# Kernel tuning notes

Measured on AMD Instinct MI355X. Metric: run time of the kernel, lower is better.

The kernel has to match this reference:

```python
import jax, jax.numpy as jnp
import numpy as np

D_K = 64  # hardcoded in source module

def setup_inputs() -> dict:
    key = jax.random.key(0)
    kq, kk, kv, km = jax.random.split(key, 4)
    B, H, S, D = 4, 16, 2048, D_K
    Q = jax.random.normal(kq, (B, H, S, D), dtype=jnp.float32)
    K = jax.random.normal(kk, (B, H, S, D), dtype=jnp.float32)
    V = jax.random.normal(kv, (B, H, S, D), dtype=jnp.float32)
    attn_mask = jax.random.randint(km, (B, H, S, S), 0, 2).astype(jnp.bool_)
    return {"Q": Q, "K": K, "V": V, "attn_mask": attn_mask}

def reference(Q, K, V, attn_mask):
    # scores: [B, H, len_q, len_k]
    scores = jnp.einsum("bhqd,bhkd->bhqk", Q, K) / np.sqrt(D_K).astype(np.float32)
    scores = jnp.where(attn_mask, jnp.float32(-1e9), scores)
    attn = jax.nn.softmax(scores, axis=-1)
    prob = jnp.einsum("bhqk,bhkd->bhqd", attn, V)
    return prob, attn
```

## Files before the change

### kernel.cpp

```cpp
#include <hip/hip_runtime.h>
#include <stdint.h>

typedef _Float16 f16;
typedef _Float16 f16x8 __attribute__((ext_vector_type(8)));
typedef _Float16 f16x4 __attribute__((ext_vector_type(4)));
typedef float f32x4 __attribute__((ext_vector_type(4)));
typedef int int4v __attribute__((ext_vector_type(4)));
typedef float float4v __attribute__((ext_vector_type(4)));

#define S_LEN 2048
#define D_DIM 64
#define QBLK 128
#define KBLK 64
#define NTHREADS 512
#define KSTEPS 32

#define BARRIER() do { \
    asm volatile("s_waitcnt lgkmcnt(0)" ::: "memory"); \
    __builtin_amdgcn_s_barrier(); \
    asm volatile("" ::: "memory"); \
} while (0)

__device__ __forceinline__ f16x8 cvt8(float4v a, float4v b) {
    f16x8 f;
    f[0]=(f16)a[0]; f[1]=(f16)a[1]; f[2]=(f16)a[2]; f[3]=(f16)a[3];
    f[4]=(f16)b[0]; f[5]=(f16)b[1]; f[6]=(f16)b[2]; f[7]=(f16)b[3];
    return f;
}
__device__ __forceinline__ uint32_t f16b(float x) {
    union { f16 h; uint16_t u; } c; c.h = (f16)x; return c.u;
}

#define S1_BODY(T, MREG) do { \
    const int tt = ((T) + phase) & 31; \
    const int cur = (T) & 1; \
    BARRIER(); \
    uint32_t bits = 0; \
    _Pragma("unroll") \
    for (int ct = 0; ct < 4; ++ct) { \
        _Pragma("unroll") \
        for (int r = 0; r < 4; ++r) \
            bits |= (MREG[ct][r] != 0 ? 1u : 0u) << (4 * ct + r); \
    } \
    if ((T) + 1 < KSTEPS) {    \
        const int tn = ((T) + 1 + phase) & 31; \
        const float* kp = kbase + (size_t)(tn * KBLK + srow) * D_DIM + scol; \
        ka = *(const float4v*)kp; kb = *(const float4v*)(kp + 4); \
    } \
    if ((T) + 2 < KSTEPS) {    \
        const int tm = ((T) + 2 + phase) & 31; \
        _Pragma("unroll") \
        for (int ct = 0; ct < 4; ++ct) \
            MREG[ct] = __builtin_nontemporal_load( \
                (const int4v*)(mbase + (size_t)tm * KBLK + 16 * ct)); \
    } \
    f32x4 c[4]; \
    _Pragma("unroll") \
    for (int ct = 0; ct < 4; ++ct) { \
        c[ct] = (f32x4){0.f, 0.f, 0.f, 0.f}; \
        _Pragma("unroll") \
        for (int h = 0; h < 2; ++h) { \
            int rowl = 16 * ct + lr; \
            int idx = (rowl * D_DIM + 8 * g + 32 * h) ^ ((rowl & 7) << 3); \
            f16x8 kf = *(const f16x8*)(&Klds[cur][idx]); \
            c[ct] = __builtin_amdgcn_mfma_f32_16x16x32_f16(kf, qfrag[h], c[ct], 0, 0, 0); \
        } \
    } \
    Mw[tt][tid] = (uint16_t)bits; \
    _Pragma("unroll") \
    for (int ct = 0; ct < 4; ++ct) { \
        _Pragma("unroll") \
        for (int r = 0; r < 4; ++r) { \
            float s = c[ct][r] * 0.125f; \
            float p = ((bits >> (4 * ct + r)) & 1) ? 0.f : __expf(s);  \
            lacc[r] += p; \
        } \
    } \
    if ((T) + 1 < KSTEPS) \
        *(f16x8*)&Klds[cur ^ 1][sidx] = cvt8(ka, kb); \
} while (0)

__global__ __launch_bounds__(NTHREADS, 4)
void sdpa_kernel(const float* __restrict__ Qg, const float* __restrict__ Kg,
                 const float* __restrict__ Vg, const int* __restrict__ Mg,
                 float* __restrict__ ProbOut, float* __restrict__ AttnOut)
{
    __shared__ f16 Klds[2][KBLK * D_DIM];
    __shared__ f16 Vtlds[2][D_DIM * KBLK];
    __shared__ uint16_t Mw[KSTEPS][NTHREADS];

    const int tid  = threadIdx.x;
    const int lane = tid & 63;
    const int wq   = tid >> 6;
    const int g    = lane >> 4;
    const int lr   = lane & 15;

    const int wid = ((blockIdx.x & 7) << 7) + (blockIdx.x >> 3);
    const int bh  = wid >> 4;
    const int qb  = wid & 15;
    const int phase = ((bh & 3) << 3) | ((qb & 1) << 2);

    const size_t qkv_base = (size_t)bh * S_LEN * D_DIM;
    const size_t mat_base = (size_t)bh * S_LEN * S_LEN;
    const int qw0 = qb * QBLK + wq * 16;

    f16x8 qfrag[2];
    {
        const float* qp = Qg + qkv_base + (size_t)(qw0 + lr) * D_DIM + g * 8;
        #pragma unroll
        for (int h = 0; h < 2; ++h)
            qfrag[h] = cvt8(*(const float4v*)(qp + 32 * h),
                            *(const float4v*)(qp + 32 * h + 4));
    }

    const int srow = tid >> 3, scol = (tid & 7) * 8;
    const int sidx = (srow * D_DIM + scol) ^ ((srow & 7) << 3);
    const int vrp  = tid >> 4, vdb = (tid & 15) * 4;
    const int vk   = 2 * vrp;
    const int vkp  = (vk & 3) | (((vk >> 4) & 3) << 2) | (((vk >> 2) & 3) << 4);

    const float* kbase = Kg + qkv_base;
    const float* vbase = Vg + qkv_base;
    const int*   mbase = Mg + mat_base + (size_t)(qw0 + lr) * S_LEN + 4 * g;

    float lacc[4] = {0.f, 0.f, 0.f, 0.f};

    float4v ka, kb;
    int4v mregA[4], mregB[4];
    {
        const float* kp = kbase + (size_t)(phase * KBLK + srow) * D_DIM + scol;
        ka = *(const float4v*)kp; kb = *(const float4v*)(kp + 4);
        const int t1 = (phase + 1) & 31;
        #pragma unroll
        for (int ct = 0; ct < 4; ++ct) {
            mregA[ct] = __builtin_nontemporal_load(
                (const int4v*)(mbase + (size_t)phase * KBLK + 16 * ct));
            mregB[ct] = __builtin_nontemporal_load(
                (const int4v*)(mbase + (size_t)t1 * KBLK + 16 * ct));
        }
    }
    *(f16x8*)&Klds[0][sidx] = cvt8(ka, kb);

    for (int t2 = 0; t2 < KSTEPS; t2 += 2) {
        S1_BODY(t2, mregA);
        S1_BODY(t2 + 1, mregB);
    }

    float lsum = (lacc[0] + lacc[1]) + (lacc[2] + lacc[3]);
    lsum += __shfl_xor(lsum, 16, 64);
    lsum += __shfl_xor(lsum, 32, 64);
    const float inv_l = 1.f / lsum;

    f32x4 acc[4];
    #pragma unroll
    for (int dt = 0; dt < 4; ++dt) acc[dt] = (f32x4){0.f, 0.f, 0.f, 0.f};

    float4v va, vb;
    {
        const float* kp = kbase + (size_t)(phase * KBLK + srow) * D_DIM + scol;
        ka = *(const float4v*)kp; kb = *(const float4v*)(kp + 4);
        const float* vp = vbase + (size_t)(phase * KBLK + vk) * D_DIM + vdb;
        va = *(const float4v*)vp; vb = *(const float4v*)(vp + D_DIM);
    }
    *(f16x8*)&Klds[0][sidx] = cvt8(ka, kb);
    #pragma unroll
    for (int j = 0; j < 4; ++j) {
        int d = vdb + j;
        uint32_t pk = f16b(va[j]) | (f16b(vb[j]) << 16);
        *(uint32_t*)&Vtlds[0][(d * KBLK + vkp) ^ ((d & 7) << 3)] = pk;
    }

    for (int t = 0; t < KSTEPS; ++t) {
        const int tt  = (t + phase) & 31;
        const int cur = t & 1;
        BARRIER();
        if (t + 1 < KSTEPS) {
            const int tn = (t + 1 + phase) & 31;
            const float* kp = kbase + (size_t)(tn * KBLK + srow) * D_DIM + scol;
            ka = *(const float4v*)kp; kb = *(const float4v*)(kp + 4);
            const float* vp = vbase + (size_t)(tn * KBLK + vk) * D_DIM + vdb;
            va = *(const float4v*)vp; vb = *(const float4v*)(vp + D_DIM);
        }
        f32x4 c[4];
        #pragma unroll
        for (int ct = 0; ct < 4; ++ct) {
            c[ct] = (f32x4){0.f, 0.f, 0.f, 0.f};
            #pragma unroll
            for (int h = 0; h < 2; ++h) {
                int rowl = 16 * ct + lr;
                int idx = (rowl * D_DIM + 8 * g + 32 * h) ^ ((rowl & 7) << 3);
                f16x8 kf = *(const f16x8*)(&Klds[cur][idx]);
                c[ct] = __builtin_amdgcn_mfma_f32_16x16x32_f16(kf, qfrag[h], c[ct], 0, 0, 0);
            }
        }
        const uint32_t bits = Mw[tt][tid];
        f16x4 pa[4];
        #pragma unroll
        for (int ct = 0; ct < 4; ++ct) {
            float4v av;
            #pragma unroll
            for (int r = 0; r < 4; ++r) {
                float s = c[ct][r] * 0.125f;
                float p = ((bits >> (4 * ct + r)) & 1) ? 0.f : __expf(s);
                float pn = p * inv_l;
                av[r] = pn; pa[ct][r] = (f16)pn;
            }
            __builtin_nontemporal_store(av,
                (float4v*)(AttnOut + mat_base + (size_t)(qw0 + lr) * S_LEN
                           + tt * KBLK + 16 * ct + 4 * g));
        }
        #pragma unroll
        for (int dt = 0; dt < 4; ++dt) {
            int row = 16 * dt + lr;
            f16x8 vfA = *(const f16x8*)&Vtlds[cur][(row * KBLK + 16 * g)      ^ ((lr & 7) << 3)];
            f16x8 vfB = *(const f16x8*)&Vtlds[cur][(row * KBLK + 16 * g + 8)  ^ ((lr & 7) << 3)];
            acc[dt] = __builtin_amdgcn_mfma_f32_16x16x16f16(
                pa[0], __builtin_shufflevector(vfA, vfA, 0, 1, 2, 3), acc[dt], 0, 0, 0);
            acc[dt] = __builtin_amdgcn_mfma_f32_16x16x16f16(
                pa[1], __builtin_shufflevector(vfA, vfA, 4, 5, 6, 7), acc[dt], 0, 0, 0);
            acc[dt] = __builtin_amdgcn_mfma_f32_16x16x16f16(
                pa[2], __builtin_shufflevector(vfB, vfB, 0, 1, 2, 3), acc[dt], 0, 0, 0);
            acc[dt] = __builtin_amdgcn_mfma_f32_16x16x16f16(
                pa[3], __builtin_shufflevector(vfB, vfB, 4, 5, 6, 7), acc[dt], 0, 0, 0);
        }
        if (t + 1 < KSTEPS) {
            *(f16x8*)&Klds[cur ^ 1][sidx] = cvt8(ka, kb);
            #pragma unroll
            for (int j = 0; j < 4; ++j) {
                int d = vdb + j;
                uint32_t pk = f16b(va[j]) | (f16b(vb[j]) << 16);
                *(uint32_t*)&Vtlds[cur ^ 1][(d * KBLK + vkp) ^ ((d & 7) << 3)] = pk;
            }
        }
    }

    #pragma unroll
    for (int dt = 0; dt < 4; ++dt) {
        #pragma unroll
        for (int r = 0; r < 4; ++r) {
            int qrow = qw0 + 4 * g + r;
            ProbOut[qkv_base + (size_t)qrow * D_DIM + 16 * dt + lr] = acc[dt][r];
        }
    }
}

extern "C" void kernel_launch(void* const* d_in, const int* in_sizes, int n_in,
                              void* d_out, int out_size, void* d_ws, size_t ws_size,
                              hipStream_t stream)
{
    const float* Q = (const float*)d_in[0];
    const float* K = (const float*)d_in[1];
    const float* V = (const float*)d_in[2];
    const int*   M = (const int*)d_in[3];

    float* prob = (float*)d_out;
    float* attn = prob + (size_t)4 * 16 * 2048 * 64;

    dim3 grid(64 * (S_LEN / QBLK));
    dim3 block(NTHREADS);
    sdpa_kernel<<<grid, block, 0, stream>>>(Q, K, V, M, prob, attn);
}
```

Baseline: 585.4 us.

## Halve Q block, load K fragments directly from global and drop K LDS staging

Shrinks the workgroup to 4 waves and 64 query rows, so there are twice as many blocks, and remaps the block-to-(bh,qb) swizzle and phase. Each wave now loads its K MFMA fragments straight from global memory and converts them in registers. This removes the shared K double buffer and the barriers in the first softmax-sum pass. The risk is redundant K global traffic across waves and blocks, which must be absorbed by L2/L1, and more per-thread V loading in the second pass.

```diff
diff --git a/kernel.cpp b/kernel.cpp
--- a/kernel.cpp
+++ b/kernel.cpp
@@ -10,9 +10,9 @@
 
 #define S_LEN 2048
 #define D_DIM 64
-#define QBLK 128
+#define QBLK 64
 #define KBLK 64
-#define NTHREADS 512
+#define NTHREADS 256
 #define KSTEPS 32
 
 #define BARRIER() do { \
@@ -31,10 +31,36 @@
     union { f16 h; uint16_t u; } c; c.h = (f16)x; return c.u;
 }
 
+#define QKT_DIRECT(C, K0) do { \
+    _Pragma("unroll") \
+    for (int half = 0; half < 2; ++half) { \
+        float4v kr[8]; \
+        _Pragma("unroll") \
+        for (int cc = 0; cc < 2; ++cc) { \
+            _Pragma("unroll") \
+            for (int h = 0; h < 2; ++h) { \
+                const float* kp = kbase + (size_t)((K0) + 16 * (2 * half + cc) + lr) * D_DIM \
+                                  + 8 * g + 32 * h; \
+                kr[(cc << 2) | (h << 1)]     = *(const float4v*)kp; \
+                kr[(cc << 2) | (h << 1) | 1] = *(const float4v*)(kp + 4); \
+            } \
+        } \
+        _Pragma("unroll") \
+        for (int cc = 0; cc < 2; ++cc) { \
+            const int ct = 2 * half + cc; \
+            C[ct] = (f32x4){0.f, 0.f, 0.f, 0.f}; \
+            _Pragma("unroll") \
+            for (int h = 0; h < 2; ++h) { \
+                f16x8 kf = cvt8(kr[(cc << 2) | (h << 1)], kr[(cc << 2) | (h << 1) | 1]); \
+                C[ct] = __builtin_amdgcn_mfma_f32_16x16x32_f16(kf, qfrag[h], C[ct], 0, 0, 0); \
+            } \
+        } \
+    } \
+} while (0)
+
 #define S1_BODY(T, MREG) do { \
     const int tt = ((T) + phase) & 31; \
-    const int cur = (T) & 1; \
-    BARRIER(); \
+    const int k0 = tt * KBLK; \
     uint32_t bits = 0; \
     _Pragma("unroll") \
     for (int ct = 0; ct < 4; ++ct) { \
@@ -42,30 +68,8 @@
         for (int r = 0; r < 4; ++r) \
             bits |= (MREG[ct][r] != 0 ? 1u : 0u) << (4 * ct + r); \
     } \
-    if ((T) + 1 < KSTEPS) {    \
-        const int tn = ((T) + 1 + phase) & 31; \
-        const float* kp = kbase + (size_t)(tn * KBLK + srow) * D_DIM + scol; \
-        ka = *(const float4v*)kp; kb = *(const float4v*)(kp + 4); \
-    } \
-    if ((T) + 2 < KSTEPS) {    \
-        const int tm = ((T) + 2 + phase) & 31; \
-        _Pragma("unroll") \
-        for (int ct = 0; ct < 4; ++ct) \
-            MREG[ct] = __builtin_nontemporal_load( \
-                (const int4v*)(mbase + (size_t)tm * KBLK + 16 * ct)); \
-    } \
     f32x4 c[4]; \
-    _Pragma("unroll") \
-    for (int ct = 0; ct < 4; ++ct) { \
-        c[ct] = (f32x4){0.f, 0.f, 0.f, 0.f}; \
-        _Pragma("unroll") \
-        for (int h = 0; h < 2; ++h) { \
-            int rowl = 16 * ct + lr; \
-            int idx = (rowl * D_DIM + 8 * g + 32 * h) ^ ((rowl & 7) << 3); \
-            f16x8 kf = *(const f16x8*)(&Klds[cur][idx]); \
-            c[ct] = __builtin_amdgcn_mfma_f32_16x16x32_f16(kf, qfrag[h], c[ct], 0, 0, 0); \
-        } \
-    } \
+    QKT_DIRECT(c, k0); \
     Mw[tt][tid] = (uint16_t)bits; \
     _Pragma("unroll") \
     for (int ct = 0; ct < 4; ++ct) { \
@@ -76,8 +80,13 @@
             lacc[r] += p; \
         } \
     } \
-    if ((T) + 1 < KSTEPS) \
-        *(f16x8*)&Klds[cur ^ 1][sidx] = cvt8(ka, kb); \
+    if ((T) + 2 < KSTEPS) {    \
+        const int tm = ((T) + 2 + phase) & 31; \
+        _Pragma("unroll") \
+        for (int ct = 0; ct < 4; ++ct) \
+            MREG[ct] = __builtin_nontemporal_load( \
+                (const int4v*)(mbase + (size_t)tm * KBLK + 16 * ct)); \
+    } \
 } while (0)
 
 __global__ __launch_bounds__(NTHREADS, 4)
@@ -85,7 +94,6 @@
                  const float* __restrict__ Vg, const int* __restrict__ Mg,
                  float* __restrict__ ProbOut, float* __restrict__ AttnOut)
 {
-    __shared__ f16 Klds[2][KBLK * D_DIM];
     __shared__ f16 Vtlds[2][D_DIM * KBLK];
     __shared__ uint16_t Mw[KSTEPS][NTHREADS];
 
@@ -95,10 +103,10 @@
     const int g    = lane >> 4;
     const int lr   = lane & 15;
 
-    const int wid = ((blockIdx.x & 7) << 7) + (blockIdx.x >> 3);
-    const int bh  = wid >> 4;
-    const int qb  = wid & 15;
-    const int phase = ((bh & 3) << 3) | ((qb & 1) << 2);
+    const int wid = ((blockIdx.x & 7) << 8) | (blockIdx.x >> 3);
+    const int bh  = wid >> 5;
+    const int qb  = wid & 31;
+    const int phase = ((bh & 3) << 3) | ((qb & 3) << 1);
 
     const size_t qkv_base = (size_t)bh * S_LEN * D_DIM;
     const size_t mat_base = (size_t)bh * S_LEN * S_LEN;
@@ -113,11 +121,10 @@
                             *(const float4v*)(qp + 32 * h + 4));
     }
 
-    const int srow = tid >> 3, scol = (tid & 7) * 8;
-    const int sidx = (srow * D_DIM + scol) ^ ((srow & 7) << 3);
-    const int vrp  = tid >> 4, vdb = (tid & 15) * 4;
-    const int vk   = 2 * vrp;
-    const int vkp  = (vk & 3) | (((vk >> 4) & 3) << 2) | (((vk >> 2) & 3) << 4);
+    const int vrp = tid >> 3;
+    const int vdb = (tid & 7) * 8;
+    const int vk  = 2 * vrp;
+    const int vkp = (vk & 3) | (((vk >> 4) & 3) << 2) | (((vk >> 2) & 3) << 4);
 
     const float* kbase = Kg + qkv_base;
     const float* vbase = Vg + qkv_base;
@@ -125,11 +132,8 @@
 
     float lacc[4] = {0.f, 0.f, 0.f, 0.f};
 
-    float4v ka, kb;
     int4v mregA[4], mregB[4];
     {
-        const float* kp = kbase + (size_t)(phase * KBLK + srow) * D_DIM + scol;
-        ka = *(const float4v*)kp; kb = *(const float4v*)(kp + 4);
         const int t1 = (phase + 1) & 31;
         #pragma unroll
         for (int ct = 0; ct < 4; ++ct) {
@@ -139,7 +143,6 @@
                 (const int4v*)(mbase + (size_t)t1 * KBLK + 16 * ct));
         }
     }
-    *(f16x8*)&Klds[0][sidx] = cvt8(ka, kb);
 
     for (int t2 = 0; t2 < KSTEPS; t2 += 2) {
         S1_BODY(t2, mregA);
@@ -155,44 +158,37 @@
     #pragma unroll
     for (int dt = 0; dt < 4; ++dt) acc[dt] = (f32x4){0.f, 0.f, 0.f, 0.f};
 
-    float4v va, vb;
+    float4v va0, va1, vb0, vb1;
     {
-        const float* kp = kbase + (size_t)(phase * KBLK + srow) * D_DIM + scol;
-        ka = *(const float4v*)kp; kb = *(const float4v*)(kp + 4);
         const float* vp = vbase + (size_t)(phase * KBLK + vk) * D_DIM + vdb;
-        va = *(const float4v*)vp; vb = *(const float4v*)(vp + D_DIM);
-    }
-    *(f16x8*)&Klds[0][sidx] = cvt8(ka, kb);
+        va0 = *(const float4v*)vp;        va1 = *(const float4v*)(vp + 4);
+        vb0 = *(const float4v*)(vp + 64); vb1 = *(const float4v*)(vp + 68);
+    }
     #pragma unroll
-    for (int j = 0; j < 4; ++j) {
+    for (int j = 0; j < 8; ++j) {
         int d = vdb + j;
-        uint32_t pk = f16b(va[j]) | (f16b(vb[j]) << 16);
+        float x0 = j < 4 ? va0[j & 3] : va1[j & 3];
+        float x1 = j < 4 ? vb0[j & 3] : vb1[j & 3];
+        uint32_t pk = f16b(x0) | (f16b(x1) << 16);
         *(uint32_t*)&Vtlds[0][(d * KBLK + vkp) ^ ((d & 7) << 3)] = pk;
     }
 
     for (int t = 0; t < KSTEPS; ++t) {
         const int tt  = (t + phase) & 31;
+        const int k0  = tt * KBLK;
         const int cur = t & 1;
         BARRIER();
+
+        f32x4 c[4];
+        QKT_DIRECT(c, k0);
+
         if (t + 1 < KSTEPS) {
             const int tn = (t + 1 + phase) & 31;
-            const float* kp = kbase + (size_t)(tn * KBLK + srow) * D_DIM + scol;
-            ka = *(const float4v*)kp; kb = *(const float4v*)(kp + 4);
             const float* vp = vbase + (size_t)(tn * KBLK + vk) * D_DIM + vdb;
-            va = *(const float4v*)vp; vb = *(const float4v*)(vp + D_DIM);
-        }
-        f32x4 c[4];
-        #pragma unroll
-        for (int ct = 0; ct < 4; ++ct) {
-            c[ct] = (f32x4){0.f, 0.f, 0.f, 0.f};
-            #pragma unroll
-            for (int h = 0; h < 2; ++h) {
-                int rowl = 16 * ct + lr;
-                int idx = (rowl * D_DIM + 8 * g + 32 * h) ^ ((rowl & 7) << 3);
-                f16x8 kf = *(const f16x8*)(&Klds[cur][idx]);
-                c[ct] = __builtin_amdgcn_mfma_f32_16x16x32_f16(kf, qfrag[h], c[ct], 0, 0, 0);
-            }
-        }
+            va0 = *(const float4v*)vp;        va1 = *(const float4v*)(vp + 4);
+            vb0 = *(const float4v*)(vp + 64); vb1 = *(const float4v*)(vp + 68);
+        }
+
         const uint32_t bits = Mw[tt][tid];
         f16x4 pa[4];
         #pragma unroll
@@ -212,8 +208,8 @@
         #pragma unroll
         for (int dt = 0; dt < 4; ++dt) {
             int row = 16 * dt + lr;
-            f16x8 vfA = *(const f16x8*)&Vtlds[cur][(row * KBLK + 16 * g)      ^ ((lr & 7) << 3)];
-            f16x8 vfB = *(const f16x8*)&Vtlds[cur][(row * KBLK + 16 * g + 8)  ^ ((lr & 7) << 3)];
+            f16x8 vfA = *(const f16x8*)&Vtlds[cur][(row * KBLK + 16 * g)     ^ ((lr & 7) << 3)];
+            f16x8 vfB = *(const f16x8*)&Vtlds[cur][(row * KBLK + 16 * g + 8) ^ ((lr & 7) << 3)];
             acc[dt] = __builtin_amdgcn_mfma_f32_16x16x16f16(
                 pa[0], __builtin_shufflevector(vfA, vfA, 0, 1, 2, 3), acc[dt], 0, 0, 0);
             acc[dt] = __builtin_amdgcn_mfma_f32_16x16x16f16(
@@ -224,11 +220,12 @@
                 pa[3], __builtin_shufflevector(vfB, vfB, 4, 5, 6, 7), acc[dt], 0, 0, 0);
         }
         if (t + 1 < KSTEPS) {
-            *(f16x8*)&Klds[cur ^ 1][sidx] = cvt8(ka, kb);
             #pragma unroll
-            for (int j = 0; j < 4; ++j) {
+            for (int j = 0; j < 8; ++j) {
                 int d = vdb + j;
-                uint32_t pk = f16b(va[j]) | (f16b(vb[j]) << 16);
+                float x0 = j < 4 ? va0[j & 3] : va1[j & 3];
+                float x1 = j < 4 ? vb0[j & 3] : vb1[j & 3];
+                uint32_t pk = f16b(x0) | (f16b(x1) << 16);
                 *(uint32_t*)&Vtlds[cur ^ 1][(d * KBLK + vkp) ^ ((d & 7) << 3)] = pk;
             }
         }
```

After: 1.281 ms. 119% more time.

## Coalesce mask loads, spill mask bits to output scratch, stage attention stores in LDS

Applied to the files above, without the earlier changes.

Mask loads now read 16 rows with a lane-contiguous int2 pattern and pack them into bits via shuffles, instead of strided per-fragment int4 loads. The packed mask bits for each pair of K tiles are temporarily written into the AttnOut buffer, in a region that is overwritten later, which frees the Mw LDS array. In the second pass, normalized probabilities are staged in an LDS buffer as f16 and written out as full 512-byte row segments every two tiles. This aims to improve coalescing of the dominant mask reads and attention writes. It adds shuffle overhead and a global round trip for the mask bits, and the attention values now pass through f16 before being stored as f32, which loses precision.

```diff
diff --git a/kernel.cpp b/kernel.cpp
--- a/kernel.cpp
+++ b/kernel.cpp
@@ -5,7 +5,7 @@
 typedef _Float16 f16x8 __attribute__((ext_vector_type(8)));
 typedef _Float16 f16x4 __attribute__((ext_vector_type(4)));
 typedef float f32x4 __attribute__((ext_vector_type(4)));
-typedef int int4v __attribute__((ext_vector_type(4)));
+typedef int int2v __attribute__((ext_vector_type(2)));
 typedef float float4v __attribute__((ext_vector_type(4)));
 
 #define S_LEN 2048
@@ -31,54 +31,22 @@
     union { f16 h; uint16_t u; } c; c.h = (f16)x; return c.u;
 }
 
-#define S1_BODY(T, MREG) do { \
-    const int tt = ((T) + phase) & 31; \
-    const int cur = (T) & 1; \
-    BARRIER(); \
-    uint32_t bits = 0; \
+#define QKT_LDS(C, CUR) do { \
     _Pragma("unroll") \
     for (int ct = 0; ct < 4; ++ct) { \
-        _Pragma("unroll") \
-        for (int r = 0; r < 4; ++r) \
-            bits |= (MREG[ct][r] != 0 ? 1u : 0u) << (4 * ct + r); \
-    } \
-    if ((T) + 1 < KSTEPS) {    \
-        const int tn = ((T) + 1 + phase) & 31; \
-        const float* kp = kbase + (size_t)(tn * KBLK + srow) * D_DIM + scol; \
-        ka = *(const float4v*)kp; kb = *(const float4v*)(kp + 4); \
-    } \
-    if ((T) + 2 < KSTEPS) {    \
-        const int tm = ((T) + 2 + phase) & 31; \
-        _Pragma("unroll") \
-        for (int ct = 0; ct < 4; ++ct) \
-            MREG[ct] = __builtin_nontemporal_load( \
-                (const int4v*)(mbase + (size_t)tm * KBLK + 16 * ct)); \
-    } \
-    f32x4 c[4]; \
-    _Pragma("unroll") \
-    for (int ct = 0; ct < 4; ++ct) { \
-        c[ct] = (f32x4){0.f, 0.f, 0.f, 0.f}; \
+        C[ct] = (f32x4){0.f, 0.f, 0.f, 0.f}; \
         _Pragma("unroll") \
         for (int h = 0; h < 2; ++h) { \
             int rowl = 16 * ct + lr; \
             int idx = (rowl * D_DIM + 8 * g + 32 * h) ^ ((rowl & 7) << 3); \
-            f16x8 kf = *(const f16x8*)(&Klds[cur][idx]); \
-            c[ct] = __builtin_amdgcn_mfma_f32_16x16x32_f16(kf, qfrag[h], c[ct], 0, 0, 0); \
-        } \
-    } \
-    Mw[tt][tid] = (uint16_t)bits; \
-    _Pragma("unroll") \
-    for (int ct = 0; ct < 4; ++ct) { \
-        _Pragma("unroll") \
-        for (int r = 0; r < 4; ++r) { \
-            float s = c[ct][r] * 0.125f; \
-            float p = ((bits >> (4 * ct + r)) & 1) ? 0.f : __expf(s);  \
-            lacc[r] += p; \
-        } \
-    } \
-    if ((T) + 1 < KSTEPS) \
-        *(f16x8*)&Klds[cur ^ 1][sidx] = cvt8(ka, kb); \
-} while (0)
+            f16x8 kf = *(const f16x8*)(&Klds[CUR][idx]); \
+            C[ct] = __builtin_amdgcn_mfma_f32_16x16x32_f16(kf, qfrag[h], C[ct], 0, 0, 0); \
+        } \
+    } \
+} while (0)
+
+#define BITSADDR(G) ((uint32_t*)(AttnOut + mat_base + \
+    (size_t)(qb * QBLK + 4 * (G) + (tid >> 7)) * S_LEN + ttl + (tid & 127)))
 
 __global__ __launch_bounds__(NTHREADS, 4)
 void sdpa_kernel(const float* __restrict__ Qg, const float* __restrict__ Kg,
@@ -87,7 +55,7 @@
 {
     __shared__ f16 Klds[2][KBLK * D_DIM];
     __shared__ f16 Vtlds[2][D_DIM * KBLK];
-    __shared__ uint16_t Mw[KSTEPS][NTHREADS];
+    __shared__ f16 Astage[8][16 * 128];
 
     const int tid  = threadIdx.x;
     const int lane = tid & 63;
@@ -98,11 +66,12 @@
     const int wid = ((blockIdx.x & 7) << 7) + (blockIdx.x >> 3);
     const int bh  = wid >> 4;
     const int qb  = wid & 15;
-    const int phase = ((bh & 3) << 3) | ((qb & 1) << 2);
+    const int phase = ((bh & 3) << 3) | ((qb & 3) << 1);
 
     const size_t qkv_base = (size_t)bh * S_LEN * D_DIM;
     const size_t mat_base = (size_t)bh * S_LEN * S_LEN;
     const int qw0 = qb * QBLK + wq * 16;
+    const int ttl = ((30 + phase) & 31) * KBLK;
 
     f16x8 qfrag[2];
     {
@@ -121,118 +90,218 @@
 
     const float* kbase = Kg + qkv_base;
     const float* vbase = Vg + qkv_base;
-    const int*   mbase = Mg + mat_base + (size_t)(qw0 + lr) * S_LEN + 4 * g;
 
     float lacc[4] = {0.f, 0.f, 0.f, 0.f};
-
     float4v ka, kb;
-    int4v mregA[4], mregB[4];
+    int2v mr[16];
+    uint32_t bitsCur = 0;
+
     {
         const float* kp = kbase + (size_t)(phase * KBLK + srow) * D_DIM + scol;
         ka = *(const float4v*)kp; kb = *(const float4v*)(kp + 4);
-        const int t1 = (phase + 1) & 31;
         #pragma unroll
-        for (int ct = 0; ct < 4; ++ct) {
-            mregA[ct] = __builtin_nontemporal_load(
-                (const int4v*)(mbase + (size_t)phase * KBLK + 16 * ct));
-            mregB[ct] = __builtin_nontemporal_load(
-                (const int4v*)(mbase + (size_t)t1 * KBLK + 16 * ct));
-        }
+        for (int i = 0; i < 16; ++i)
+            mr[i] = __builtin_nontemporal_load(
+                (const int2v*)(Mg + mat_base + (size_t)(qw0 + i) * S_LEN
+                               + phase * KBLK + 2 * lane));
+        *(f16x8*)&Klds[0][sidx] = cvt8(ka, kb);
     }
-    *(f16x8*)&Klds[0][sidx] = cvt8(ka, kb);
-
-    for (int t2 = 0; t2 < KSTEPS; t2 += 2) {
-        S1_BODY(t2, mregA);
-        S1_BODY(t2 + 1, mregB);
-    }
+
+#define S1E(T) do { \
+    BARRIER(); \
+     \
+    uint32_t nib = 0; \
+    _Pragma("unroll") \
+    for (int i = 0; i < 16; ++i) \
+        nib |= ((mr[i][0] != 0 ? 1u : 0u) | (mr[i][1] != 0 ? 2u : 0u)) << (2 * i); \
+     \
+    uint32_t bits0 = 0, bits1 = 0; \
+    _Pragma("unroll") \
+    for (int ct = 0; ct < 4; ++ct) { \
+        _Pragma("unroll") \
+        for (int rp = 0; rp < 2; ++rp) { \
+            int s0 = 8 * ct + 2 * g + rp; \
+            uint32_t n0 = (uint32_t)__shfl((int)nib, s0, 64); \
+            uint32_t n1 = (uint32_t)__shfl((int)nib, s0 + 32, 64); \
+            bits0 |= ((n0 >> (2 * lr)) & 3u) << (4 * ct + 2 * rp); \
+            bits1 |= ((n1 >> (2 * lr)) & 3u) << (4 * ct + 2 * rp); \
+        } \
+    } \
+    bitsCur = bits0 | (bits1 << 16); \
+    *BITSADDR((T) >> 1) = bitsCur; \
+    if ((T) + 1 < KSTEPS) { \
+        const int tn = ((T) + 1 + phase) & 31; \
+        const float* kp = kbase + (size_t)(tn * KBLK + srow) * D_DIM + scol; \
+        ka = *(const float4v*)kp; kb = *(const float4v*)(kp + 4); \
+    } \
+    f32x4 c[4]; \
+    QKT_LDS(c, (T) & 1); \
+    _Pragma("unroll") \
+    for (int ct = 0; ct < 4; ++ct) { \
+        _Pragma("unroll") \
+        for (int r = 0; r < 4; ++r) { \
+            float s = c[ct][r] * 0.125f; \
+            float p = ((bitsCur >> (4 * ct + r)) & 1) ? 0.f : __expf(s);  \
+            lacc[r] += p; \
+        } \
+    } \
+    if ((T) + 1 < KSTEPS) *(f16x8*)&Klds[((T) & 1) ^ 1][sidx] = cvt8(ka, kb); \
+} while (0)
+
+#define S1O(T) do { \
+    BARRIER(); \
+    if ((T) + 1 < KSTEPS) { \
+        const int tn = ((T) + 1 + phase) & 31; \
+        const float* kp = kbase + (size_t)(tn * KBLK + srow) * D_DIM + scol; \
+        ka = *(const float4v*)kp; kb = *(const float4v*)(kp + 4); \
+        _Pragma("unroll") \
+        for (int i = 0; i < 16; ++i)    \
+            mr[i] = __builtin_nontemporal_load( \
+                (const int2v*)(Mg + mat_base + (size_t)(qw0 + i) * S_LEN \
+                               + tn * KBLK + 2 * lane)); \
+    } \
+    f32x4 c[4]; \
+    QKT_LDS(c, (T) & 1); \
+    { uint32_t b1 = bitsCur >> 16; \
+      _Pragma("unroll") \
+      for (int ct = 0; ct < 4; ++ct) { \
+          _Pragma("unroll") \
+          for (int r = 0; r < 4; ++r) { \
+              float s = c[ct][r] * 0.125f; \
+              float p = ((b1 >> (4 * ct + r)) & 1) ? 0.f : __expf(s); \
+              lacc[r] += p; \
+          } \
+      } } \
+    if ((T) + 1 < KSTEPS) *(f16x8*)&Klds[((T) & 1) ^ 1][sidx] = cvt8(ka, kb); \
+} while (0)
+
+    S1E(0);  S1O(1);  S1E(2);  S1O(3);  S1E(4);  S1O(5);  S1E(6);  S1O(7);
+    S1E(8);  S1O(9);  S1E(10); S1O(11); S1E(12); S1O(13); S1E(14); S1O(15);
+    S1E(16); S1O(17); S1E(18); S1O(19); S1E(20); S1O(21); S1E(22); S1O(23);
+    S1E(24); S1O(25); S1E(26); S1O(27); S1E(28); S1O(29); S1E(30); S1O(31);
 
     float lsum = (lacc[0] + lacc[1]) + (lacc[2] + lacc[3]);
     lsum += __shfl_xor(lsum, 16, 64);
     lsum += __shfl_xor(lsum, 32, 64);
     const float inv_l = 1.f / lsum;
 
+    asm volatile("s_waitcnt vmcnt(0)" ::: "memory");
+    __syncthreads();
+
     f32x4 acc[4];
     #pragma unroll
     for (int dt = 0; dt < 4; ++dt) acc[dt] = (f32x4){0.f, 0.f, 0.f, 0.f};
 
     float4v va, vb;
+    uint32_t buCur, buNxt = 0;
     {
         const float* kp = kbase + (size_t)(phase * KBLK + srow) * D_DIM + scol;
         ka = *(const float4v*)kp; kb = *(const float4v*)(kp + 4);
         const float* vp = vbase + (size_t)(phase * KBLK + vk) * D_DIM + vdb;
         va = *(const float4v*)vp; vb = *(const float4v*)(vp + D_DIM);
-    }
-    *(f16x8*)&Klds[0][sidx] = cvt8(ka, kb);
-    #pragma unroll
-    for (int j = 0; j < 4; ++j) {
-        int d = vdb + j;
-        uint32_t pk = f16b(va[j]) | (f16b(vb[j]) << 16);
-        *(uint32_t*)&Vtlds[0][(d * KBLK + vkp) ^ ((d & 7) << 3)] = pk;
-    }
-
-    for (int t = 0; t < KSTEPS; ++t) {
-        const int tt  = (t + phase) & 31;
-        const int cur = t & 1;
-        BARRIER();
-        if (t + 1 < KSTEPS) {
-            const int tn = (t + 1 + phase) & 31;
-            const float* kp = kbase + (size_t)(tn * KBLK + srow) * D_DIM + scol;
-            ka = *(const float4v*)kp; kb = *(const float4v*)(kp + 4);
-            const float* vp = vbase + (size_t)(tn * KBLK + vk) * D_DIM + vdb;
-            va = *(const float4v*)vp; vb = *(const float4v*)(vp + D_DIM);
-        }
-        f32x4 c[4];
+        buCur = *BITSADDR(0);
+        *(f16x8*)&Klds[0][sidx] = cvt8(ka, kb);
         #pragma unroll
-        for (int ct = 0; ct < 4; ++ct) {
-            c[ct] = (f32x4){0.f, 0.f, 0.f, 0.f};
-            #pragma unroll
-            for (int h = 0; h < 2; ++h) {
-                int rowl = 16 * ct + lr;
-                int idx = (rowl * D_DIM + 8 * g + 32 * h) ^ ((rowl & 7) << 3);
-                f16x8 kf = *(const f16x8*)(&Klds[cur][idx]);
-                c[ct] = __builtin_amdgcn_mfma_f32_16x16x32_f16(kf, qfrag[h], c[ct], 0, 0, 0);
-            }
-        }
-        const uint32_t bits = Mw[tt][tid];
-        f16x4 pa[4];
-        #pragma unroll
-        for (int ct = 0; ct < 4; ++ct) {
-            float4v av;
-            #pragma unroll
-            for (int r = 0; r < 4; ++r) {
-                float s = c[ct][r] * 0.125f;
-                float p = ((bits >> (4 * ct + r)) & 1) ? 0.f : __expf(s);
-                float pn = p * inv_l;
-                av[r] = pn; pa[ct][r] = (f16)pn;
-            }
-            __builtin_nontemporal_store(av,
-                (float4v*)(AttnOut + mat_base + (size_t)(qw0 + lr) * S_LEN
-                           + tt * KBLK + 16 * ct + 4 * g));
-        }
-        #pragma unroll
-        for (int dt = 0; dt < 4; ++dt) {
-            int row = 16 * dt + lr;
-            f16x8 vfA = *(const f16x8*)&Vtlds[cur][(row * KBLK + 16 * g)      ^ ((lr & 7) << 3)];
-            f16x8 vfB = *(const f16x8*)&Vtlds[cur][(row * KBLK + 16 * g + 8)  ^ ((lr & 7) << 3)];
-            acc[dt] = __builtin_amdgcn_mfma_f32_16x16x16f16(
-                pa[0], __builtin_shufflevector(vfA, vfA, 0, 1, 2, 3), acc[dt], 0, 0, 0);
-            acc[dt] = __builtin_amdgcn_mfma_f32_16x16x16f16(
-                pa[1], __builtin_shufflevector(vfA, vfA, 4, 5, 6, 7), acc[dt], 0, 0, 0);
-            acc[dt] = __builtin_amdgcn_mfma_f32_16x16x16f16(
-                pa[2], __builtin_shufflevector(vfB, vfB, 0, 1, 2, 3), acc[dt], 0, 0, 0);
-            acc[dt] = __builtin_amdgcn_mfma_f32_16x16x16f16(
-                pa[3], __builtin_shufflevector(vfB, vfB, 4, 5, 6, 7), acc[dt], 0, 0, 0);
-        }
-        if (t + 1 < KSTEPS) {
-            *(f16x8*)&Klds[cur ^ 1][sidx] = cvt8(ka, kb);
-            #pragma unroll
-            for (int j = 0; j < 4; ++j) {
-                int d = vdb + j;
-                uint32_t pk = f16b(va[j]) | (f16b(vb[j]) << 16);
-                *(uint32_t*)&Vtlds[cur ^ 1][(d * KBLK + vkp) ^ ((d & 7) << 3)] = pk;
-            }
+        for (int j = 0; j < 4; ++j) {
+            int d = vdb + j;
+            *(uint32_t*)&Vtlds[0][(d * KBLK + vkp) ^ ((d & 7) << 3)] =
+                f16b(va[j]) | (f16b(vb[j]) << 16);
         }
     }
+
+#define S2_CORE(T, BITS, PAR) do { \
+    f32x4 c[4]; \
+    QKT_LDS(c, (T) & 1); \
+    f16x4 pa[4]; \
+    _Pragma("unroll") \
+    for (int ct = 0; ct < 4; ++ct) { \
+        float av[4]; \
+        _Pragma("unroll") \
+        for (int r = 0; r < 4; ++r) { \
+            float s = c[ct][r] * 0.125f; \
+            float p = ((BITS) >> (4 * ct + r) & 1) ? 0.f : __expf(s); \
+            av[r] = p * inv_l; pa[ct][r] = (f16)av[r]; \
+        } \
+        _Pragma("unroll") \
+        for (int u = 0; u < 2; ++u) { \
+            int col = 64 * (PAR) + 16 * ct + 4 * g + 2 * u; \
+            int idx = (lr * 128 + col) ^ ((lr & 7) << 3); \
+            *(uint32_t*)&Astage[wq][idx] = f16b(av[2 * u]) | (f16b(av[2 * u + 1]) << 16); \
+        } \
+    } \
+    _Pragma("unroll") \
+    for (int dt = 0; dt < 4; ++dt) { \
+        int row = 16 * dt + lr; \
+        f16x8 vfA = *(const f16x8*)&Vtlds[(T) & 1][(row * KBLK + 16 * g)     ^ ((lr & 7) << 3)]; \
+        f16x8 vfB = *(const f16x8*)&Vtlds[(T) & 1][(row * KBLK + 16 * g + 8) ^ ((lr & 7) << 3)]; \
+        acc[dt] = __builtin_amdgcn_mfma_f32_16x16x16f16( \
+            pa[0], __builtin_shufflevector(vfA, vfA, 0, 1, 2, 3), acc[dt], 0, 0, 0); \
+        acc[dt] = __builtin_amdgcn_mfma_f32_16x16x16f16( \
+            pa[1], __builtin_shufflevector(vfA, vfA, 4, 5, 6, 7), acc[dt], 0, 0, 0); \
+        acc[dt] = __builtin_amdgcn_mfma_f32_16x16x16f16( \
+            pa[2], __builtin_shufflevector(vfB, vfB, 0, 1, 2, 3), acc[dt], 0, 0, 0); \
+        acc[dt] = __builtin_amdgcn_mfma_f32_16x16x16f16( \
+            pa[3], __builtin_shufflevector(vfB, vfB, 4, 5, 6, 7), acc[dt], 0, 0, 0); \
+    } \
+} while (0)
+
+#define S2_LOADS(T) do { \
+    if ((T) + 1 < KSTEPS) { \
+        const int tn = ((T) + 1 + phase) & 31; \
+        const float* kp = kbase + (size_t)(tn * KBLK + srow) * D_DIM + scol; \
+        ka = *(const float4v*)kp; kb = *(const float4v*)(kp + 4); \
+        const float* vp = vbase + (size_t)(tn * KBLK + vk) * D_DIM + vdb; \
+        va = *(const float4v*)vp; vb = *(const float4v*)(vp + D_DIM); \
+    } \
+} while (0)
+
+#define S2_STAGE(T) do { \
+    if ((T) + 1 < KSTEPS) { \
+        *(f16x8*)&Klds[((T) & 1) ^ 1][sidx] = cvt8(ka, kb); \
+        _Pragma("unroll") \
+        for (int j = 0; j < 4; ++j) { \
+            int d = vdb + j; \
+            *(uint32_t*)&Vtlds[((T) & 1) ^ 1][(d * KBLK + vkp) ^ ((d & 7) << 3)] = \
+                f16b(va[j]) | (f16b(vb[j]) << 16); \
+        } \
+    } \
+} while (0)
+
+#define STORE_GROUP(TE) do { \
+    const int ttp = ((TE) + phase) & 31; \
+    _Pragma("unroll") \
+    for (int i = 0; i < 8; ++i) { \
+        int row = 2 * i + (lane >> 5); \
+        int cf  = 4 * (lane & 31); \
+        int idx = (row * 128 + cf) ^ ((row & 7) << 3); \
+        f16x4 a = *(const f16x4*)&Astage[wq][idx]; \
+        float4v o; o[0]=(float)a[0]; o[1]=(float)a[1]; o[2]=(float)a[2]; o[3]=(float)a[3]; \
+        __builtin_nontemporal_store(o, (float4v*)(AttnOut + mat_base + \
+            (size_t)(qw0 + row) * S_LEN + ttp * KBLK + cf)); \
+    } \
+} while (0)
+
+#define S2E(T) do { \
+    BARRIER(); \
+    S2_LOADS(T); \
+    if ((T) + 2 < KSTEPS) buNxt = *BITSADDR(((T) >> 1) + 1); \
+    S2_CORE(T, buCur & 0xffffu, 0); \
+    S2_STAGE(T); \
+} while (0)
+
+#define S2O(T) do { \
+    BARRIER(); \
+    S2_LOADS(T); \
+    S2_CORE(T, buCur >> 16, 1); \
+    S2_STAGE(T); \
+    STORE_GROUP((T) - 1); \
+    buCur = buNxt; \
+} while (0)
+
+    S2E(0);  S2O(1);  S2E(2);  S2O(3);  S2E(4);  S2O(5);  S2E(6);  S2O(7);
+    S2E(8);  S2O(9);  S2E(10); S2O(11); S2E(12); S2O(13); S2E(14); S2O(15);
+    S2E(16); S2O(17); S2E(18); S2O(19); S2E(20); S2O(21); S2E(22); S2O(23);
+    S2E(24); S2O(25); S2E(26); S2O(27); S2E(28); S2O(29); S2E(30); S2O(31);
 
     #pragma unroll
     for (int dt = 0; dt < 4; ++dt) {
```

After: 637.5 us. 1.09x slower.
